# Kernel tuning notes

Hardware: AMD Instinct MI355X
Metric: run time of the kernel (lower is better)

## Reference

```python
import jax, jax.numpy as jnp
import numpy as np

D_MODEL, D_STATE, B, S = 1024, 64, 8, 2048


def setup_inputs() -> dict:
    key = jax.random.key(0)
    ks = jax.random.split(key, 14)
    inp = {"x": jax.random.normal(ks[0], (B, S, D_MODEL), jnp.float32)}
    names = ["cog", "beh", "env", "delta", "Bp", "Cp"]
    for i, n in enumerate(names):
        inp[f"W_{n}"] = jax.random.normal(ks[1 + 2 * i], (D_STATE, D_MODEL), jnp.float32) / np.sqrt(D_MODEL)
        inp[f"b_{n}"] = jnp.zeros((D_STATE,), jnp.float32)
    # torch init is log(|randn|+1e-4); we use strictly-negative A_log so the
    # length-2048 multiplicative recurrence stays finite (A_log is a learned
    # parameter, so its value is free; the math of forward is unchanged).
    inp["A_log"] = -jnp.abs(jax.random.normal(ks[13], (D_STATE, D_STATE), jnp.float32)) - 0.1
    return inp


def reference(x, W_cog, b_cog, W_beh, b_beh, W_env, b_env,
              W_delta, b_delta, W_Bp, b_Bp, W_Cp, b_Cp, A_log):
    # gating terms (computed in the source but never used downstream)
    A_t = (jax.nn.sigmoid(x @ W_cog.T + b_cog)
           * jax.nn.sigmoid(x @ W_beh.T + b_beh)
           * jax.nn.sigmoid(x @ W_env.T + b_env))
    del A_t

    delta = jax.nn.softplus(x @ W_delta.T + b_delta)   # [B,S,N]
    Bt = x @ W_Bp.T + b_Bp                             # [B,S,N]
    Ct = x @ W_Cp.T + b_Cp                             # [B,S,N]
    u = Bt * x[:, :, :D_STATE]                         # [B,S,N]

    # Faithful to torch broadcasting: after step 0 the carried state h is
    # [B,N,N] with h[b,i,j] = exp(A_log[i,j]*delta[b,t,i]) * h_prev[b,i,j] + u[b,t,j]
    def step(h, td):
        d, u_t, c_t = td                               # each [B,N]
        A = jnp.exp(A_log[None, :, :] * d[:, :, None]) # [B,N,N]
        h = A * h + u_t[:, None, :]
        y = jnp.einsum('bj,bij->bi', c_t, h)           # [B,N]
        return h, y

    h0 = jnp.zeros((x.shape[0], D_STATE, D_STATE), x.dtype)
    _, ys = jax.lax.scan(
        step, h0,
        (delta.transpose(1, 0, 2), u.transpose(1, 0, 2), Ct.transpose(1, 0, 2)))
    # torch stacks y_t of shape [B,1,N] along dim=1 -> [B,S,1,N]
    return ys.transpose(1, 0, 2)[:, :, None, :]
```

## Files before the change

### kernel.cpp

```cpp
#include <hip/hip_runtime.h>
#include <math.h>

#define DM   1024
#define DS   64
#define BATCH 8
#define SEQ  2048
#define CL   32
#define NC   64

typedef __bf16 bf16x8 __attribute__((ext_vector_type(8)));
typedef float  f32x4  __attribute__((ext_vector_type(4)));

#if __has_builtin(__builtin_amdgcn_exp2f)
#define EXP2(v) __builtin_amdgcn_exp2f(v)
#else
#define EXP2(v) __expf(0.69314718056f * (v))
#endif

__global__ __launch_bounds__(256) void wconv_kernel(
    const float* __restrict__ Wd, const float* __restrict__ Wb,
    const float* __restrict__ Wc, __bf16* __restrict__ Wp)
{
    int idx = blockIdx.x * 256 + threadIdx.x;
    int k  = idx & 1023;
    int n  = idx >> 10;
    const float* W = (n < 64) ? Wd : (n < 128 ? Wb : Wc);
    float v = W[(size_t)(n & 63) * DM + k];
    int kt = k >> 5, kk = k & 31;
    Wp[((size_t)kt * 192 + n) * 32 + kk] = (__bf16)v;
}

__global__ __launch_bounds__(256, 2) void projp1_full(
    const float* __restrict__ x, const __bf16* __restrict__ Wp,
    const float* __restrict__ bd, const float* __restrict__ bb,
    const float* __restrict__ bc, const float* __restrict__ A_log,
    float* __restrict__ delta_g, float* __restrict__ u_g,
    float* __restrict__ ct_g,
    float* __restrict__ E, float* __restrict__ Dsum)
{
    __shared__ __bf16 sA[4][32 * 72];
    __shared__ float  s_d[CL * 64];
    __shared__ float  s_u[CL * 64];

    const int tid  = threadIdx.x;
    const int row0 = blockIdx.x * 32;

    const int lane = tid & 63, wv = tid >> 6;
    const int l15  = lane & 15, quad = lane >> 4;
    const int nbase = wv * 48;

    const int am = tid >> 3;
    const int ak = tid & 7;
    const float* xga = x + (size_t)(row0 + am) * DM + ak * 8;

    const __bf16* wpb = Wp + (nbase + l15) * 32 + quad * 8;

    f32x4 acc[2][3];
    #pragma unroll
    for (int mt = 0; mt < 2; ++mt)
        #pragma unroll
        for (int nt = 0; nt < 3; ++nt)
            acc[mt][nt] = (f32x4){0.f, 0.f, 0.f, 0.f};

    float4 areg[4];
    bf16x8 bA[6], bB[6];

    #define LOADA2(pp) do {                                                   \
        areg[0] = *(const float4*)(xga + (pp) * 128);                         \
        areg[1] = *(const float4*)(xga + (pp) * 128 + 4);                     \
        areg[2] = *(const float4*)(xga + (pp) * 128 + 64);                    \
        areg[3] = *(const float4*)(xga + (pp) * 128 + 68);                    \
    } while (0)
    #define STAGEA2(be, bo) do {                                              \
        bf16x8 h0 = {(__bf16)areg[0].x, (__bf16)areg[0].y,                    \
                     (__bf16)areg[0].z, (__bf16)areg[0].w,                    \
                     (__bf16)areg[1].x, (__bf16)areg[1].y,                    \
                     (__bf16)areg[1].z, (__bf16)areg[1].w};                   \
        *(bf16x8*)&sA[be][am * 72 + ak * 8] = h0;                             \
        bf16x8 h1 = {(__bf16)areg[2].x, (__bf16)areg[2].y,                    \
                     (__bf16)areg[2].z, (__bf16)areg[2].w,                    \
                     (__bf16)areg[3].x, (__bf16)areg[3].y,                    \
                     (__bf16)areg[3].z, (__bf16)areg[3].w};                   \
        *(bf16x8*)&sA[bo][am * 72 + ak * 8] = h1;                             \
    } while (0)
    #define LOADBF(dst, kb) do {                                              \
        const __bf16* wb_ = wpb + (size_t)(kb) * 12288;                       \
        dst[0] = *(const bf16x8*)(wb_);                                       \
        dst[1] = *(const bf16x8*)(wb_ + 512);                                 \
        dst[2] = *(const bf16x8*)(wb_ + 1024);                                \
        dst[3] = *(const bf16x8*)(wb_ + 6144);                                \
        dst[4] = *(const bf16x8*)(wb_ + 6656);                                \
        dst[5] = *(const bf16x8*)(wb_ + 7168);                                \
    } while (0)
    #define COMPUTE(bi, bfr) do {                                             \
        _Pragma("unroll")                                                     \
        for (int s = 0; s < 2; ++s) {                                         \
            bf16x8 af0 = *(const bf16x8*)                                     \
                &sA[bi][(l15) * 72 + s * 32 + quad * 8];                      \
            bf16x8 af1 = *(const bf16x8*)                                     \
                &sA[bi][(16 + l15) * 72 + s * 32 + quad * 8];                 \
            _Pragma("unroll")                                                 \
            for (int nt = 0; nt < 3; ++nt) {                                  \
                acc[0][nt] = __builtin_amdgcn_mfma_f32_16x16x32_bf16(         \
                    af0, bfr[s * 3 + nt], acc[0][nt], 0, 0, 0);               \
                acc[1][nt] = __builtin_amdgcn_mfma_f32_16x16x32_bf16(         \
                    af1, bfr[s * 3 + nt], acc[1][nt], 0, 0, 0);               \
            }                                                                 \
        }                                                                     \
    } while (0)

    LOADA2(0);
    STAGEA2(0, 1);
    LOADA2(1);
    LOADBF(bA, 0);
    __syncthreads();

    for (int p = 0; p < 8; ++p) {
        const int pe = (p & 1) * 2, po = pe + 1;
        LOADBF(bB, 2 * p + 1);
        COMPUTE(pe, bA);
        if (p < 7) STAGEA2(pe ^ 2, po ^ 2);
        if (p < 6) LOADA2(p + 2);
        if (p < 7) LOADBF(bA, 2 * p + 2);
        COMPUTE(po, bB);
        __syncthreads();
    }
    #undef LOADA2
    #undef STAGEA2
    #undef LOADBF
    #undef COMPUTE

    #pragma unroll
    for (int nt = 0; nt < 3; ++nt) {
        int gn  = nbase + nt * 16 + l15;
        int mat = (nbase + nt * 16) >> 6;
        int col = gn & 63;
        float bias = (mat == 0) ? bd[col] : (mat == 1 ? bb[col] : bc[col]);
        #pragma unroll
        for (int mt = 0; mt < 2; ++mt) {
            #pragma unroll
            for (int r = 0; r < 4; ++r) {
                int tl = mt * 16 + quad * 4 + r;
                int m  = row0 + tl;
                float v = acc[mt][nt][r] + bias;
                if (mat == 0) {
                    float sp = (v > 20.f) ? v : __logf(1.f + __expf(v));
                    delta_g[(size_t)m * DS + col] = sp;
                    s_d[tl * 64 + col] = sp;
                } else if (mat == 1) {
                    float uu = v * x[(size_t)m * DM + col];
                    u_g[(size_t)m * DS + col] = uu;
                    s_u[tl * 64 + col] = uu;
                } else {
                    ct_g[(size_t)m * DS + col] = v;
                }
            }
        }
    }
    __syncthreads();

    const int bidx = row0 >> 11;
    const int cidx = (row0 >> 5) & 63;
    const int si = tid & 63;
    const int sj = tid >> 6;

    float alog[16];
    {
        const float4* ar = (const float4*)(A_log + si * 64 + sj * 16);
        #pragma unroll
        for (int qq = 0; qq < 4; ++qq) {
            float4 v = ar[qq];
            alog[4*qq+0] = v.x * 1.44269504f; alog[4*qq+1] = v.y * 1.44269504f;
            alog[4*qq+2] = v.z * 1.44269504f; alog[4*qq+3] = v.w * 1.44269504f;
        }
    }

    float h[16];
    #pragma unroll
    for (int k = 0; k < 16; ++k) h[k] = 0.f;
    float dsum = 0.f;

    for (int t = 0; t < CL; ++t) {
        float d = s_d[t * 64 + si];
        dsum += d;
        const float* up = s_u + t * 64 + sj * 16;
        #pragma unroll
        for (int k = 0; k < 16; ++k)
            h[k] = EXP2(alog[k] * d) * h[k] + up[k];
    }

    float* eo = E + (((size_t)cidx * BATCH + bidx) * 64 + si) * 64 + sj * 16;
    #pragma unroll
    for (int qq = 0; qq < 4; ++qq)
        ((float4*)eo)[qq] = make_float4(h[4*qq], h[4*qq+1], h[4*qq+2], h[4*qq+3]);
    if (sj == 0) Dsum[((size_t)cidx * BATCH + bidx) * 64 + si] = dsum;
}

__device__ __forceinline__ void scan_range(
    const float* __restrict__ Eb, const float* __restrict__ Db,
    int n0, int n1, int bb_, int i_, int jg_,
    const float* __restrict__ alog, float* __restrict__ h)
{
    if (n0 >= n1) return;
    size_t idx = ((size_t)n0 * BATCH + bb_) * 64 + i_;
    float dsA = Db[idx];
    const float4* ep = (const float4*)(Eb + idx * 64 + jg_ * 16);
    float4 e0 = ep[0], e1 = ep[1], e2 = ep[2], e3 = ep[3];
    for (int n = n0; n < n1; ++n) {
        float dsN = 0.f;
        float4 f0 = make_float4(0.f,0.f,0.f,0.f), f1 = f0, f2 = f0, f3 = f0;
        if (n + 1 < n1) {
            size_t idx2 = ((size_t)(n + 1) * BATCH + bb_) * 64 + i_;
            dsN = Db[idx2];
            const float4* fp = (const float4*)(Eb + idx2 * 64 + jg_ * 16);
            f0 = fp[0]; f1 = fp[1]; f2 = fp[2]; f3 = fp[3];
        }
        float ev[16] = {e0.x,e0.y,e0.z,e0.w, e1.x,e1.y,e1.z,e1.w,
                        e2.x,e2.y,e2.z,e2.w, e3.x,e3.y,e3.z,e3.w};
        #pragma unroll
        for (int k = 0; k < 16; ++k)
            h[k] = EXP2(alog[k] * dsA) * h[k] + ev[k];
        dsA = dsN; e0 = f0; e1 = f1; e2 = f2; e3 = f3;
    }
}

__global__ __launch_bounds__(256) void group_kernel(
    const float* __restrict__ E, const float* __restrict__ Dsum,
    const float* __restrict__ A_log,
    float* __restrict__ Eg, float* __restrict__ Dg)
{
    const int g2 = blockIdx.x >> 3, b2 = blockIdx.x & 7;
    const int tid = threadIdx.x;
    const int i  = tid >> 2;
    const int jg = tid & 3;

    float alog[16];
    {
        const float4* ar = (const float4*)(A_log + i * 64 + jg * 16);
        #pragma unroll
        for (int qq = 0; qq < 4; ++qq) {
            float4 v = ar[qq];
            alog[4*qq+0] = v.x * 1.44269504f; alog[4*qq+1] = v.y * 1.44269504f;
            alog[4*qq+2] = v.z * 1.44269504f; alog[4*qq+3] = v.w * 1.44269504f;
        }
    }

    float hg[16];
    #pragma unroll
    for (int k = 0; k < 16; ++k) hg[k] = 0.f;
    scan_range(E, Dsum, g2 * 8, g2 * 8 + 8, b2, i, jg, alog, hg);

    float4* ego = (float4*)(Eg + (((size_t)g2 * BATCH + b2) * 64 + i) * 64 + jg * 16);
    ego[0] = make_float4(hg[0],  hg[1],  hg[2],  hg[3]);
    ego[1] = make_float4(hg[4],  hg[5],  hg[6],  hg[7]);
    ego[2] = make_float4(hg[8],  hg[9],  hg[10], hg[11]);
    ego[3] = make_float4(hg[12], hg[13], hg[14], hg[15]);
    if (jg == 0) {
        float Dacc = 0.f;
        #pragma unroll
        for (int q = 0; q < 8; ++q)
            Dacc += Dsum[((size_t)(g2 * 8 + q) * BATCH + b2) * 64 + i];
        Dg[((size_t)g2 * BATCH + b2) * 64 + i] = Dacc;
    }
}

__global__ __launch_bounds__(256) void pass23_kernel(
    const float* __restrict__ delta_g, const float* __restrict__ u_g,
    const float* __restrict__ ct_g, const float* __restrict__ A_log,
    const float* __restrict__ E, const float* __restrict__ Dsum,
    const float* __restrict__ Eg, const float* __restrict__ Dg,
    float* __restrict__ out)
{
    __shared__ float s_d[CL * 64];
    __shared__ float s_u[CL * 64];
    __shared__ float s_c[CL * 64];

    const int c = blockIdx.x, b = blockIdx.y, tid = threadIdx.x;
    const int t0 = c * CL;

    const float4* dg = (const float4*)(delta_g + ((size_t)b * SEQ + t0) * DS);
    const float4* ug = (const float4*)(u_g     + ((size_t)b * SEQ + t0) * DS);
    const float4* cg = (const float4*)(ct_g    + ((size_t)b * SEQ + t0) * DS);
    #pragma unroll
    for (int it = 0; it < (CL * 64 / 4) / 256; ++it) {
        int f = tid + it * 256;
        ((float4*)s_d)[f] = dg[f];
        ((float4*)s_u)[f] = ug[f];
        ((float4*)s_c)[f] = cg[f];
    }

    const int i  = tid >> 2;
    const int jg = tid & 3;

    float alog[16];
    {
        const float4* ar = (const float4*)(A_log + i * 64 + jg * 16);
        #pragma unroll
        for (int qq = 0; qq < 4; ++qq) {
            float4 v = ar[qq];
            alog[4*qq+0] = v.x * 1.44269504f; alog[4*qq+1] = v.y * 1.44269504f;
            alog[4*qq+2] = v.z * 1.44269504f; alog[4*qq+3] = v.w * 1.44269504f;
        }
    }

    float h[16];
    #pragma unroll
    for (int k = 0; k < 16; ++k) h[k] = 0.f;
    const int g = c >> 3;
    scan_range(Eg, Dg, 0, g, b, i, jg, alog, h);
    scan_range(E, Dsum, g * 8, c, b, i, jg, alog, h);
    __syncthreads();

    for (int t = 0; t < CL; ++t) {
        float d = s_d[t * 64 + i];
        const float* up  = s_u + t * 64 + jg * 16;
        const float* cp2 = s_c + t * 64 + jg * 16;
        float part = 0.f;
        #pragma unroll
        for (int k = 0; k < 16; ++k) {
            h[k] = EXP2(alog[k] * d) * h[k] + up[k];
            part += cp2[k] * h[k];
        }
        part += __shfl_xor(part, 1);
        part += __shfl_xor(part, 2);
        if (jg == 0)
            out[((size_t)b * SEQ + t0 + t) * DS + i] = part;
    }
}

extern "C" void kernel_launch(void* const* d_in, const int* in_sizes, int n_in,
                              void* d_out, int out_size, void* d_ws, size_t ws_size,
                              hipStream_t stream)
{
    (void)in_sizes; (void)n_in; (void)out_size; (void)ws_size;
    const float* x     = (const float*)d_in[0];
    const float* Wd    = (const float*)d_in[7];
    const float* bd    = (const float*)d_in[8];
    const float* Wb    = (const float*)d_in[9];
    const float* bb    = (const float*)d_in[10];
    const float* Wc    = (const float*)d_in[11];
    const float* bc    = (const float*)d_in[12];
    const float* A_log = (const float*)d_in[13];
    float* out = (float*)d_out;

    float* ws = (float*)d_ws;
    float* delta_g = ws;
    float* u_g     = ws + 1 * 1048576;
    float* ct_g    = ws + 2 * 1048576;
    float* E       = ws + 3 * 1048576;
    float* Dsum    = ws + 5242880;
    float* Eg      = ws + 5275648;
    float* Dg      = ws + 5537792;
    __bf16* Wp     = (__bf16*)(ws + 5541888);

    wconv_kernel<<<768, 256, 0, stream>>>(Wd, Wb, Wc, Wp);
    projp1_full<<<512, 256, 0, stream>>>(
        x, Wp, bd, bb, bc, A_log, delta_g, u_g, ct_g, E, Dsum);
    group_kernel<<<64, 256, 0, stream>>>(E, Dsum, A_log, Eg, Dg);
    pass23_kernel<<<dim3(NC, BATCH), 256, 0, stream>>>(
        delta_g, u_g, ct_g, A_log, E, Dsum, Eg, Dg, out);
}
```

Baseline: 170.3 us.

## Fuse all stages into one persistent kernel with grid-wide barriers

Merges the weight conversion, projection GEMM, chunk scan, group scan and final output pass into a single persistent kernel of 512 blocks, separated by atomic-counter grid barriers. Delta, u and C stay in shared memory between the projection and output phases, so the three per-token intermediate arrays are never written to and re-read from global memory. This removes three kernel launches and that traffic. In exchange it adds a memset, spin-wait barriers whose correctness depends on all 512 blocks being co-resident, and a group phase in which only 64 blocks do work while the rest wait.

```diff
diff --git a/kernel.cpp b/kernel.cpp
--- a/kernel.cpp
+++ b/kernel.cpp
@@ -7,6 +7,7 @@
 #define SEQ  2048
 #define CL   32
 #define NC   64
+#define NBLK 512
 
 typedef __bf16 bf16x8 __attribute__((ext_vector_type(8)));
 typedef float  f32x4  __attribute__((ext_vector_type(4)));
@@ -17,183 +18,26 @@
 #define EXP2(v) __expf(0.69314718056f * (v))
 #endif
 
-__global__ __launch_bounds__(256) void wconv_kernel(
-    const float* __restrict__ Wd, const float* __restrict__ Wb,
-    const float* __restrict__ Wc, __bf16* __restrict__ Wp)
+#define LBAR() do {                                                           \
+    asm volatile("s_waitcnt lgkmcnt(0)" ::: "memory");                        \
+    __builtin_amdgcn_s_barrier();                                             \
+    asm volatile("" ::: "memory");                                            \
+} while (0)
+
+__device__ __forceinline__ void gbar(unsigned* ctr)
 {
-    int idx = blockIdx.x * 256 + threadIdx.x;
-    int k  = idx & 1023;
-    int n  = idx >> 10;
-    const float* W = (n < 64) ? Wd : (n < 128 ? Wb : Wc);
-    float v = W[(size_t)(n & 63) * DM + k];
-    int kt = k >> 5, kk = k & 31;
-    Wp[((size_t)kt * 192 + n) * 32 + kk] = (__bf16)v;
-}
-
-__global__ __launch_bounds__(256, 2) void projp1_full(
-    const float* __restrict__ x, const __bf16* __restrict__ Wp,
-    const float* __restrict__ bd, const float* __restrict__ bb,
-    const float* __restrict__ bc, const float* __restrict__ A_log,
-    float* __restrict__ delta_g, float* __restrict__ u_g,
-    float* __restrict__ ct_g,
-    float* __restrict__ E, float* __restrict__ Dsum)
-{
-    __shared__ __bf16 sA[4][32 * 72];
-    __shared__ float  s_d[CL * 64];
-    __shared__ float  s_u[CL * 64];
-
-    const int tid  = threadIdx.x;
-    const int row0 = blockIdx.x * 32;
-
-    const int lane = tid & 63, wv = tid >> 6;
-    const int l15  = lane & 15, quad = lane >> 4;
-    const int nbase = wv * 48;
-
-    const int am = tid >> 3;
-    const int ak = tid & 7;
-    const float* xga = x + (size_t)(row0 + am) * DM + ak * 8;
-
-    const __bf16* wpb = Wp + (nbase + l15) * 32 + quad * 8;
-
-    f32x4 acc[2][3];
-    #pragma unroll
-    for (int mt = 0; mt < 2; ++mt)
-        #pragma unroll
-        for (int nt = 0; nt < 3; ++nt)
-            acc[mt][nt] = (f32x4){0.f, 0.f, 0.f, 0.f};
-
-    float4 areg[4];
-    bf16x8 bA[6], bB[6];
-
-    #define LOADA2(pp) do {                                                   \
-        areg[0] = *(const float4*)(xga + (pp) * 128);                         \
-        areg[1] = *(const float4*)(xga + (pp) * 128 + 4);                     \
-        areg[2] = *(const float4*)(xga + (pp) * 128 + 64);                    \
-        areg[3] = *(const float4*)(xga + (pp) * 128 + 68);                    \
-    } while (0)
-    #define STAGEA2(be, bo) do {                                              \
-        bf16x8 h0 = {(__bf16)areg[0].x, (__bf16)areg[0].y,                    \
-                     (__bf16)areg[0].z, (__bf16)areg[0].w,                    \
-                     (__bf16)areg[1].x, (__bf16)areg[1].y,                    \
-                     (__bf16)areg[1].z, (__bf16)areg[1].w};                   \
-        *(bf16x8*)&sA[be][am * 72 + ak * 8] = h0;                             \
-        bf16x8 h1 = {(__bf16)areg[2].x, (__bf16)areg[2].y,                    \
-                     (__bf16)areg[2].z, (__bf16)areg[2].w,                    \
-                     (__bf16)areg[3].x, (__bf16)areg[3].y,                    \
-                     (__bf16)areg[3].z, (__bf16)areg[3].w};                   \
-        *(bf16x8*)&sA[bo][am * 72 + ak * 8] = h1;                             \
-    } while (0)
-    #define LOADBF(dst, kb) do {                                              \
-        const __bf16* wb_ = wpb + (size_t)(kb) * 12288;                       \
-        dst[0] = *(const bf16x8*)(wb_);                                       \
-        dst[1] = *(const bf16x8*)(wb_ + 512);                                 \
-        dst[2] = *(const bf16x8*)(wb_ + 1024);                                \
-        dst[3] = *(const bf16x8*)(wb_ + 6144);                                \
-        dst[4] = *(const bf16x8*)(wb_ + 6656);                                \
-        dst[5] = *(const bf16x8*)(wb_ + 7168);                                \
-    } while (0)
-    #define COMPUTE(bi, bfr) do {                                             \
-        _Pragma("unroll")                                                     \
-        for (int s = 0; s < 2; ++s) {                                         \
-            bf16x8 af0 = *(const bf16x8*)                                     \
-                &sA[bi][(l15) * 72 + s * 32 + quad * 8];                      \
-            bf16x8 af1 = *(const bf16x8*)                                     \
-                &sA[bi][(16 + l15) * 72 + s * 32 + quad * 8];                 \
-            _Pragma("unroll")                                                 \
-            for (int nt = 0; nt < 3; ++nt) {                                  \
-                acc[0][nt] = __builtin_amdgcn_mfma_f32_16x16x32_bf16(         \
-                    af0, bfr[s * 3 + nt], acc[0][nt], 0, 0, 0);               \
-                acc[1][nt] = __builtin_amdgcn_mfma_f32_16x16x32_bf16(         \
-                    af1, bfr[s * 3 + nt], acc[1][nt], 0, 0, 0);               \
-            }                                                                 \
-        }                                                                     \
-    } while (0)
-
-    LOADA2(0);
-    STAGEA2(0, 1);
-    LOADA2(1);
-    LOADBF(bA, 0);
     __syncthreads();
-
-    for (int p = 0; p < 8; ++p) {
-        const int pe = (p & 1) * 2, po = pe + 1;
-        LOADBF(bB, 2 * p + 1);
-        COMPUTE(pe, bA);
-        if (p < 7) STAGEA2(pe ^ 2, po ^ 2);
-        if (p < 6) LOADA2(p + 2);
-        if (p < 7) LOADBF(bA, 2 * p + 2);
-        COMPUTE(po, bB);
-        __syncthreads();
-    }
-    #undef LOADA2
-    #undef STAGEA2
-    #undef LOADBF
-    #undef COMPUTE
-
-    #pragma unroll
-    for (int nt = 0; nt < 3; ++nt) {
-        int gn  = nbase + nt * 16 + l15;
-        int mat = (nbase + nt * 16) >> 6;
-        int col = gn & 63;
-        float bias = (mat == 0) ? bd[col] : (mat == 1 ? bb[col] : bc[col]);
-        #pragma unroll
-        for (int mt = 0; mt < 2; ++mt) {
-            #pragma unroll
-            for (int r = 0; r < 4; ++r) {
-                int tl = mt * 16 + quad * 4 + r;
-                int m  = row0 + tl;
-                float v = acc[mt][nt][r] + bias;
-                if (mat == 0) {
-                    float sp = (v > 20.f) ? v : __logf(1.f + __expf(v));
-                    delta_g[(size_t)m * DS + col] = sp;
-                    s_d[tl * 64 + col] = sp;
-                } else if (mat == 1) {
-                    float uu = v * x[(size_t)m * DM + col];
-                    u_g[(size_t)m * DS + col] = uu;
-                    s_u[tl * 64 + col] = uu;
-                } else {
-                    ct_g[(size_t)m * DS + col] = v;
-                }
-            }
-        }
+    if (threadIdx.x == 0) {
+        __threadfence();
+        unsigned my = __hip_atomic_fetch_add(
+            ctr, 1u, __ATOMIC_ACQ_REL, __HIP_MEMORY_SCOPE_AGENT);
+        unsigned target = my - (my % NBLK) + NBLK;
+        while (__hip_atomic_load(ctr, __ATOMIC_ACQUIRE,
+                                 __HIP_MEMORY_SCOPE_AGENT) < target)
+            __builtin_amdgcn_s_sleep(2);
+        __threadfence();
     }
     __syncthreads();
-
-    const int bidx = row0 >> 11;
-    const int cidx = (row0 >> 5) & 63;
-    const int si = tid & 63;
-    const int sj = tid >> 6;
-
-    float alog[16];
-    {
-        const float4* ar = (const float4*)(A_log + si * 64 + sj * 16);
-        #pragma unroll
-        for (int qq = 0; qq < 4; ++qq) {
-            float4 v = ar[qq];
-            alog[4*qq+0] = v.x * 1.44269504f; alog[4*qq+1] = v.y * 1.44269504f;
-            alog[4*qq+2] = v.z * 1.44269504f; alog[4*qq+3] = v.w * 1.44269504f;
-        }
-    }
-
-    float h[16];
-    #pragma unroll
-    for (int k = 0; k < 16; ++k) h[k] = 0.f;
-    float dsum = 0.f;
-
-    for (int t = 0; t < CL; ++t) {
-        float d = s_d[t * 64 + si];
-        dsum += d;
-        const float* up = s_u + t * 64 + sj * 16;
-        #pragma unroll
-        for (int k = 0; k < 16; ++k)
-            h[k] = EXP2(alog[k] * d) * h[k] + up[k];
-    }
-
-    float* eo = E + (((size_t)cidx * BATCH + bidx) * 64 + si) * 64 + sj * 16;
-    #pragma unroll
-    for (int qq = 0; qq < 4; ++qq)
-        ((float4*)eo)[qq] = make_float4(h[4*qq], h[4*qq+1], h[4*qq+2], h[4*qq+3]);
-    if (sj == 0) Dsum[((size_t)cidx * BATCH + bidx) * 64 + si] = dsum;
 }
 
 __device__ __forceinline__ void scan_range(
@@ -224,107 +68,241 @@
     }
 }
 
-__global__ __launch_bounds__(256) void group_kernel(
-    const float* __restrict__ E, const float* __restrict__ Dsum,
-    const float* __restrict__ A_log,
-    float* __restrict__ Eg, float* __restrict__ Dg)
+__global__ __launch_bounds__(256, 2) void mega_kernel(
+    const float* __restrict__ x,
+    const float* __restrict__ Wd, const float* __restrict__ Wb,
+    const float* __restrict__ Wc,
+    const float* __restrict__ bd, const float* __restrict__ bb,
+    const float* __restrict__ bc, const float* __restrict__ A_log,
+    __bf16* __restrict__ Wp,
+    float* __restrict__ E, float* __restrict__ Dsum,
+    float* __restrict__ Eg, float* __restrict__ Dg,
+    unsigned* __restrict__ ctrs,
+    float* __restrict__ out)
 {
-    const int g2 = blockIdx.x >> 3, b2 = blockIdx.x & 7;
-    const int tid = threadIdx.x;
+    __shared__ __align__(16) char smem[34816];
+    __bf16* sAb = (__bf16*)smem;
+    float*  s_c = (float*)smem;
+    float*  s_d = (float*)(smem + 18432);
+    float*  s_u = (float*)(smem + 26624);
+
+    const int tid  = threadIdx.x;
+    const int row0 = blockIdx.x * 32;
+
+    for (int idx = blockIdx.x * 256 + tid; idx < 192 * 1024; idx += NBLK * 256) {
+        int k = idx & 1023;
+        int n = idx >> 10;
+        const float* W = (n < 64) ? Wd : (n < 128 ? Wb : Wc);
+        float v = W[(size_t)(n & 63) * DM + k];
+        int kt = k >> 5, kk = k & 31;
+        Wp[((size_t)kt * 192 + n) * 32 + kk] = (__bf16)v;
+    }
+    gbar(ctrs + 0);
+
+    const int lane = tid & 63, wv = tid >> 6;
+    const int l15  = lane & 15, quad = lane >> 4;
+    const int nbase = wv * 48;
+
+    const int am = tid >> 3;
+    const int ak = tid & 7;
+    const float* xga = x + (size_t)(row0 + am) * DM + ak * 8;
+    const __bf16* wpb = Wp + (nbase + l15) * 32 + quad * 8;
+
+    f32x4 acc[2][3];
+    #pragma unroll
+    for (int mt = 0; mt < 2; ++mt)
+        #pragma unroll
+        for (int nt = 0; nt < 3; ++nt)
+            acc[mt][nt] = (f32x4){0.f, 0.f, 0.f, 0.f};
+
+    float4 areg[4];
+    bf16x8 bA[6], bB[6];
+
+    #define LOADA2(pp) do {                                                   \
+        areg[0] = *(const float4*)(xga + (pp) * 128);                         \
+        areg[1] = *(const float4*)(xga + (pp) * 128 + 4);                     \
+        areg[2] = *(const float4*)(xga + (pp) * 128 + 64);                    \
+        areg[3] = *(const float4*)(xga + (pp) * 128 + 68);                    \
+    } while (0)
+    #define STAGEA2(be, bo) do {                                              \
+        bf16x8 h0 = {(__bf16)areg[0].x, (__bf16)areg[0].y,                    \
+                     (__bf16)areg[0].z, (__bf16)areg[0].w,                    \
+                     (__bf16)areg[1].x, (__bf16)areg[1].y,                    \
+                     (__bf16)areg[1].z, (__bf16)areg[1].w};                   \
+        *(bf16x8*)&sAb[(be) * 2304 + am * 72 + ak * 8] = h0;                  \
+        bf16x8 h1 = {(__bf16)areg[2].x, (__bf16)areg[2].y,                    \
+                     (__bf16)areg[2].z, (__bf16)areg[2].w,                    \
+                     (__bf16)areg[3].x, (__bf16)areg[3].y,                    \
+                     (__bf16)areg[3].z, (__bf16)areg[3].w};                   \
+        *(bf16x8*)&sAb[(bo) * 2304 + am * 72 + ak * 8] = h1;                  \
+    } while (0)
+    #define LOADBF(dst, kb) do {                                              \
+        const __bf16* wb_ = wpb + (size_t)(kb) * 12288;                       \
+        dst[0] = *(const bf16x8*)(wb_);                                       \
+        dst[1] = *(const bf16x8*)(wb_ + 512);                                 \
+        dst[2] = *(const bf16x8*)(wb_ + 1024);                                \
+        dst[3] = *(const bf16x8*)(wb_ + 6144);                                \
+        dst[4] = *(const bf16x8*)(wb_ + 6656);                                \
+        dst[5] = *(const bf16x8*)(wb_ + 7168);                                \
+    } while (0)
+    #define COMPUTE(bi, bfr) do {                                             \
+        _Pragma("unroll")                                                     \
+        for (int s = 0; s < 2; ++s) {                                         \
+            bf16x8 af0 = *(const bf16x8*)                                     \
+                &sAb[(bi) * 2304 + (l15) * 72 + s * 32 + quad * 8];           \
+            bf16x8 af1 = *(const bf16x8*)                                     \
+                &sAb[(bi) * 2304 + (16 + l15) * 72 + s * 32 + quad * 8];      \
+            _Pragma("unroll")                                                 \
+            for (int nt = 0; nt < 3; ++nt) {                                  \
+                acc[0][nt] = __builtin_amdgcn_mfma_f32_16x16x32_bf16(         \
+                    af0, bfr[s * 3 + nt], acc[0][nt], 0, 0, 0);               \
+                acc[1][nt] = __builtin_amdgcn_mfma_f32_16x16x32_bf16(         \
+                    af1, bfr[s * 3 + nt], acc[1][nt], 0, 0, 0);               \
+            }                                                                 \
+        }                                                                     \
+    } while (0)
+
+    LOADA2(0);
+    STAGEA2(0, 1);
+    LOADA2(1);
+    LOADBF(bA, 0);
+    LBAR();
+
+    for (int p = 0; p < 8; ++p) {
+        const int pe = (p & 1) * 2, po = pe + 1;
+        LOADBF(bB, 2 * p + 1);
+        COMPUTE(pe, bA);
+        if (p < 7) STAGEA2(pe ^ 2, po ^ 2);
+        if (p < 6) LOADA2(p + 2);
+        if (p < 7) LOADBF(bA, 2 * p + 2);
+        COMPUTE(po, bB);
+        LBAR();
+    }
+    #undef LOADA2
+    #undef STAGEA2
+    #undef LOADBF
+    #undef COMPUTE
+
+    #pragma unroll
+    for (int nt = 0; nt < 3; ++nt) {
+        int gn  = nbase + nt * 16 + l15;
+        int mat = (nbase + nt * 16) >> 6;
+        int col = gn & 63;
+        float bias = (mat == 0) ? bd[col] : (mat == 1 ? bb[col] : bc[col]);
+        #pragma unroll
+        for (int mt = 0; mt < 2; ++mt) {
+            #pragma unroll
+            for (int r = 0; r < 4; ++r) {
+                int tl = mt * 16 + quad * 4 + r;
+                int m  = row0 + tl;
+                float v = acc[mt][nt][r] + bias;
+                if (mat == 0) {
+                    float sp = (v > 20.f) ? v : __logf(1.f + __expf(v));
+                    s_d[tl * 64 + col] = sp;
+                } else if (mat == 1) {
+                    s_u[tl * 64 + col] = v * x[(size_t)m * DM + col];
+                } else {
+                    s_c[tl * 64 + col] = v;
+                }
+            }
+        }
+    }
+    LBAR();
+
+    const int bidx = row0 >> 11;
+    const int cidx = (row0 >> 5) & 63;
+    {
+        const int si = tid & 63;
+        const int sj = tid >> 6;
+        float alog1[16];
+        const float4* ar = (const float4*)(A_log + si * 64 + sj * 16);
+        #pragma unroll
+        for (int qq = 0; qq < 4; ++qq) {
+            float4 v = ar[qq];
+            alog1[4*qq+0] = v.x * 1.44269504f; alog1[4*qq+1] = v.y * 1.44269504f;
+            alog1[4*qq+2] = v.z * 1.44269504f; alog1[4*qq+3] = v.w * 1.44269504f;
+        }
+        float h1[16];
+        #pragma unroll
+        for (int k = 0; k < 16; ++k) h1[k] = 0.f;
+        float dsum = 0.f;
+        for (int t = 0; t < CL; ++t) {
+            float d = s_d[t * 64 + si];
+            dsum += d;
+            const float* up = s_u + t * 64 + sj * 16;
+            #pragma unroll
+            for (int k = 0; k < 16; ++k)
+                h1[k] = EXP2(alog1[k] * d) * h1[k] + up[k];
+        }
+        float* eo = E + (((size_t)cidx * BATCH + bidx) * 64 + si) * 64 + sj * 16;
+        #pragma unroll
+        for (int qq = 0; qq < 4; ++qq)
+            ((float4*)eo)[qq] =
+                make_float4(h1[4*qq], h1[4*qq+1], h1[4*qq+2], h1[4*qq+3]);
+        if (sj == 0) Dsum[((size_t)cidx * BATCH + bidx) * 64 + si] = dsum;
+    }
+
+    gbar(ctrs + 16);
+
     const int i  = tid >> 2;
     const int jg = tid & 3;
-
     float alog[16];
     {
-        const float4* ar = (const float4*)(A_log + i * 64 + jg * 16);
+        const float4* ar2 = (const float4*)(A_log + i * 64 + jg * 16);
         #pragma unroll
         for (int qq = 0; qq < 4; ++qq) {
-            float4 v = ar[qq];
+            float4 v = ar2[qq];
             alog[4*qq+0] = v.x * 1.44269504f; alog[4*qq+1] = v.y * 1.44269504f;
             alog[4*qq+2] = v.z * 1.44269504f; alog[4*qq+3] = v.w * 1.44269504f;
         }
     }
-
-    float hg[16];
-    #pragma unroll
-    for (int k = 0; k < 16; ++k) hg[k] = 0.f;
-    scan_range(E, Dsum, g2 * 8, g2 * 8 + 8, b2, i, jg, alog, hg);
-
-    float4* ego = (float4*)(Eg + (((size_t)g2 * BATCH + b2) * 64 + i) * 64 + jg * 16);
-    ego[0] = make_float4(hg[0],  hg[1],  hg[2],  hg[3]);
-    ego[1] = make_float4(hg[4],  hg[5],  hg[6],  hg[7]);
-    ego[2] = make_float4(hg[8],  hg[9],  hg[10], hg[11]);
-    ego[3] = make_float4(hg[12], hg[13], hg[14], hg[15]);
-    if (jg == 0) {
-        float Dacc = 0.f;
-        #pragma unroll
-        for (int q = 0; q < 8; ++q)
-            Dacc += Dsum[((size_t)(g2 * 8 + q) * BATCH + b2) * 64 + i];
-        Dg[((size_t)g2 * BATCH + b2) * 64 + i] = Dacc;
-    }
-}
-
-__global__ __launch_bounds__(256) void pass23_kernel(
-    const float* __restrict__ delta_g, const float* __restrict__ u_g,
-    const float* __restrict__ ct_g, const float* __restrict__ A_log,
-    const float* __restrict__ E, const float* __restrict__ Dsum,
-    const float* __restrict__ Eg, const float* __restrict__ Dg,
-    float* __restrict__ out)
-{
-    __shared__ float s_d[CL * 64];
-    __shared__ float s_u[CL * 64];
-    __shared__ float s_c[CL * 64];
-
-    const int c = blockIdx.x, b = blockIdx.y, tid = threadIdx.x;
-    const int t0 = c * CL;
-
-    const float4* dg = (const float4*)(delta_g + ((size_t)b * SEQ + t0) * DS);
-    const float4* ug = (const float4*)(u_g     + ((size_t)b * SEQ + t0) * DS);
-    const float4* cg = (const float4*)(ct_g    + ((size_t)b * SEQ + t0) * DS);
-    #pragma unroll
-    for (int it = 0; it < (CL * 64 / 4) / 256; ++it) {
-        int f = tid + it * 256;
-        ((float4*)s_d)[f] = dg[f];
-        ((float4*)s_u)[f] = ug[f];
-        ((float4*)s_c)[f] = cg[f];
-    }
-
-    const int i  = tid >> 2;
-    const int jg = tid & 3;
-
-    float alog[16];
+    if (blockIdx.x < 64) {
+        const int g2 = blockIdx.x >> 3, b2 = blockIdx.x & 7;
+        float hg[16];
+        #pragma unroll
+        for (int k = 0; k < 16; ++k) hg[k] = 0.f;
+        scan_range(E, Dsum, g2 * 8, g2 * 8 + 8, b2, i, jg, alog, hg);
+        float4* ego = (float4*)(Eg + (((size_t)g2 * BATCH + b2) * 64 + i) * 64
+                                   + jg * 16);
+        ego[0] = make_float4(hg[0],  hg[1],  hg[2],  hg[3]);
+        ego[1] = make_float4(hg[4],  hg[5],  hg[6],  hg[7]);
+        ego[2] = make_float4(hg[8],  hg[9],  hg[10], hg[11]);
+        ego[3] = make_float4(hg[12], hg[13], hg[14], hg[15]);
+        if (jg == 0) {
+            float Dacc = 0.f;
+            #pragma unroll
+            for (int q = 0; q < 8; ++q)
+                Dacc += Dsum[((size_t)(g2 * 8 + q) * BATCH + b2) * 64 + i];
+            Dg[((size_t)g2 * BATCH + b2) * 64 + i] = Dacc;
+        }
+    }
+
+    gbar(ctrs + 32);
+
     {
-        const float4* ar = (const float4*)(A_log + i * 64 + jg * 16);
-        #pragma unroll
-        for (int qq = 0; qq < 4; ++qq) {
-            float4 v = ar[qq];
-            alog[4*qq+0] = v.x * 1.44269504f; alog[4*qq+1] = v.y * 1.44269504f;
-            alog[4*qq+2] = v.z * 1.44269504f; alog[4*qq+3] = v.w * 1.44269504f;
-        }
-    }
-
-    float h[16];
-    #pragma unroll
-    for (int k = 0; k < 16; ++k) h[k] = 0.f;
-    const int g = c >> 3;
-    scan_range(Eg, Dg, 0, g, b, i, jg, alog, h);
-    scan_range(E, Dsum, g * 8, c, b, i, jg, alog, h);
-    __syncthreads();
-
-    for (int t = 0; t < CL; ++t) {
-        float d = s_d[t * 64 + i];
-        const float* up  = s_u + t * 64 + jg * 16;
-        const float* cp2 = s_c + t * 64 + jg * 16;
-        float part = 0.f;
-        #pragma unroll
-        for (int k = 0; k < 16; ++k) {
-            h[k] = EXP2(alog[k] * d) * h[k] + up[k];
-            part += cp2[k] * h[k];
-        }
-        part += __shfl_xor(part, 1);
-        part += __shfl_xor(part, 2);
-        if (jg == 0)
-            out[((size_t)b * SEQ + t0 + t) * DS + i] = part;
+        float h[16];
+        #pragma unroll
+        for (int k = 0; k < 16; ++k) h[k] = 0.f;
+        const int g = cidx >> 3;
+        scan_range(Eg, Dg, 0, g, bidx, i, jg, alog, h);
+        scan_range(E, Dsum, g * 8, cidx, bidx, i, jg, alog, h);
+
+        const int t0 = cidx * CL;
+        for (int t = 0; t < CL; ++t) {
+            float d = s_d[t * 64 + i];
+            const float* up  = s_u + t * 64 + jg * 16;
+            const float* cp2 = s_c + t * 64 + jg * 16;
+            float part = 0.f;
+            #pragma unroll
+            for (int k = 0; k < 16; ++k) {
+                h[k] = EXP2(alog[k] * d) * h[k] + up[k];
+                part += cp2[k] * h[k];
+            }
+            part += __shfl_xor(part, 1);
+            part += __shfl_xor(part, 2);
+            if (jg == 0)
+                out[((size_t)bidx * SEQ + t0 + t) * DS + i] = part;
+        }
     }
 }
 
@@ -344,19 +322,15 @@
     float* out = (float*)d_out;
 
     float* ws = (float*)d_ws;
-    float* delta_g = ws;
-    float* u_g     = ws + 1 * 1048576;
-    float* ct_g    = ws + 2 * 1048576;
-    float* E       = ws + 3 * 1048576;
-    float* Dsum    = ws + 5242880;
-    float* Eg      = ws + 5275648;
-    float* Dg      = ws + 5537792;
-    __bf16* Wp     = (__bf16*)(ws + 5541888);
-
-    wconv_kernel<<<768, 256, 0, stream>>>(Wd, Wb, Wc, Wp);
-    projp1_full<<<512, 256, 0, stream>>>(
-        x, Wp, bd, bb, bc, A_log, delta_g, u_g, ct_g, E, Dsum);
-    group_kernel<<<64, 256, 0, stream>>>(E, Dsum, A_log, Eg, Dg);
-    pass23_kernel<<<dim3(NC, BATCH), 256, 0, stream>>>(
-        delta_g, u_g, ct_g, A_log, E, Dsum, Eg, Dg, out);
+    unsigned* ctrs = (unsigned*)ws;
+    float* E    = ws + 64;
+    float* Dsum = ws + 64 + 2097152;
+    float* Eg   = ws + 64 + 2129920;
+    float* Dg   = ws + 64 + 2392064;
+    __bf16* Wp  = (__bf16*)(ws + 64 + 2396160);
+
+    hipMemsetAsync(ctrs, 0, 256, stream);
+
+    mega_kernel<<<NBLK, 256, 0, stream>>>(
+        x, Wd, Wb, Wc, bd, bb, bc, A_log, Wp, E, Dsum, Eg, Dg, ctrs, out);
 }
```

After: 369.8 us. +117.1%, slower.
